# Kernel optimization log

Hardware: AMD Instinct MI355X
Metric: run time of the kernel (lower is better)

## Reference

```python
import jax, jax.numpy as jnp
import numpy as np

NUM_EMBEDDINGS = 1024
EMBEDDING_DIM = 256
COMMITMENT_COST = 0.25
B = 65536


def setup_inputs() -> dict:
    key = jax.random.key(0)
    k1, k2 = jax.random.split(key)
    inputs = jax.random.normal(k1, (B, EMBEDDING_DIM), dtype=jnp.float32)
    # torch init: uniform(-1/K, 1/K)
    W = jax.random.uniform(k2, (NUM_EMBEDDINGS, EMBEDDING_DIM), dtype=jnp.float32,
                           minval=-1.0 / NUM_EMBEDDINGS, maxval=1.0 / NUM_EMBEDDINGS)
    return {"inputs": inputs, "W": W}


def reference(inputs, W):
    x = inputs  # (B, D)
    # squared L2 distances to every codebook entry: (B, K)
    distances = (jnp.sum(x * x, axis=1, keepdims=True)
                 + jnp.sum(W * W, axis=1)
                 - 2.0 * jnp.matmul(x, W.T))
    idx = jnp.argmin(distances, axis=1)  # (B,)
    # one-hot @ W is just a gather
    quantized = jnp.take(W, idx, axis=0)  # (B, D)

    sg = jax.lax.stop_gradient
    e_latent_loss = jnp.mean((sg(quantized) - x) ** 2)
    q_latent_loss = jnp.mean((quantized - sg(x)) ** 2)
    loss = q_latent_loss + COMMITMENT_COST * e_latent_loss

    # perplexity from code-usage histogram (mean of one-hot rows)
    counts = jax.ops.segment_sum(jnp.ones((x.shape[0],), dtype=x.dtype), idx,
                                 num_segments=NUM_EMBEDDINGS)
    avg_probs = counts / x.shape[0]
    perplexity = jnp.exp(-jnp.sum(avg_probs * jnp.log(avg_probs + 1e-10)))

    # straight-through estimator
    quantized_st = x + sg(quantized - x)
    return quantized_st, loss, perplexity
```

## Files before the change

kernel.cpp:

```cpp
#include <hip/hip_runtime.h>


using h16   = _Float16;
using h16x8 = __attribute__((ext_vector_type(8))) _Float16;
using f32x4 = __attribute__((ext_vector_type(4))) float;

#define W_SCALE 1024.0f
#define W_UNSCALE2 0.001953125f
#define XS_STRIDE 264

__global__ __launch_bounds__(64) void vq_wconv(const float* __restrict__ W,
                                               h16* __restrict__ Whp,
                                               float* __restrict__ wws) {
  const int t = threadIdx.x;
  const int code = blockIdx.x * 2 + (t >> 5);
  const int j = t & 31;
  const int d0 = j * 8;
  f32x4 v0 = *(const f32x4*)(W + (size_t)code * 256 + d0);
  f32x4 v1 = *(const f32x4*)(W + (size_t)code * 256 + d0 + 4);
  h16x8 h;
  h[0] = (h16)(v0[0] * W_SCALE); h[1] = (h16)(v0[1] * W_SCALE);
  h[2] = (h16)(v0[2] * W_SCALE); h[3] = (h16)(v0[3] * W_SCALE);
  h[4] = (h16)(v1[0] * W_SCALE); h[5] = (h16)(v1[1] * W_SCALE);
  h[6] = (h16)(v1[2] * W_SCALE); h[7] = (h16)(v1[3] * W_SCALE);
  const int tile = code >> 4, ks = j >> 2, quad = j & 3, lm = code & 15;
  *(h16x8*)(Whp + (size_t)(((tile * 8 + ks) * 64 + quad * 16 + lm) * 8)) = h;
  float ss = v0[0] * v0[0] + v0[1] * v0[1] + v0[2] * v0[2] + v0[3] * v0[3]
           + v1[0] * v1[0] + v1[1] * v1[1] + v1[2] * v1[2] + v1[3] * v1[3];
#pragma unroll
  for (int m = 1; m <= 16; m <<= 1) ss += __shfl_xor(ss, m);
  if (j == 0) wws[code] = ss;
}

__global__ __launch_bounds__(256, 4) void vq_main(const float* __restrict__ X,
                                                  const h16* __restrict__ Whp,
                                                  const float* __restrict__ wws,
                                                  const float* __restrict__ W,
                                                  float* __restrict__ out,
                                                  float* __restrict__ loss_sum,
                                                  int* __restrict__ counts) {
  __shared__ h16 Xs[64 * XS_STRIDE];
  __shared__ float redS[4 * 64];
  __shared__ int redC[4 * 64];
  __shared__ int sIdx[64];
  __shared__ float xnorm[64];
  const int tid = threadIdx.x;
  const int lane = tid & 63;
  const int wid = tid >> 6;
  const int lm = lane & 15;
  const int quad = lane >> 4;
  const int rowBase = blockIdx.x * 64;

#pragma unroll
  for (int it = 0; it < 8; ++it) {
    int q = it * 256 + tid;
    int r = q >> 5;
    int dp = (q & 31) << 3;
    const float* src = X + (size_t)(rowBase + r) * 256 + dp;
    f32x4 v0 = __builtin_nontemporal_load((const f32x4*)src);
    f32x4 v1 = __builtin_nontemporal_load((const f32x4*)src + 1);
    h16x8 h;
    h[0] = (h16)v0[0]; h[1] = (h16)v0[1]; h[2] = (h16)v0[2]; h[3] = (h16)v0[3];
    h[4] = (h16)v1[0]; h[5] = (h16)v1[1]; h[6] = (h16)v1[2]; h[7] = (h16)v1[3];
    *(h16x8*)(Xs + r * XS_STRIDE + dp) = h;
    float ss = v0[0] * v0[0] + v0[1] * v0[1] + v0[2] * v0[2] + v0[3] * v0[3]
             + v1[0] * v1[0] + v1[1] * v1[1] + v1[2] * v1[2] + v1[3] * v1[3];
#pragma unroll
    for (int m = 1; m <= 16; m <<= 1) ss += __shfl_xor(ss, m);
    if ((q & 31) == 0) xnorm[r] = ss;
  }
  __syncthreads();

  float bestS[16];
  int bestC[16];
#pragma unroll
  for (int s = 0; s < 16; ++s) { bestS[s] = 3.4e38f; bestC[s] = 0x7fffffff; }

  for (int chunk = 0; chunk < 8; ++chunk) {
    const int tbase = chunk * 8 + wid * 2;
    const h16* bptr = Whp + (size_t)tbase * 4096 + lane * 8;
    float wn0 = wws[tbase * 16 + lm];
    float wn1 = wws[tbase * 16 + 16 + lm];
    f32x4 acc[4][2];
#pragma unroll
    for (int mt = 0; mt < 4; ++mt)
#pragma unroll
      for (int nt = 0; nt < 2; ++nt) {
        f32x4 z = {0.0f, 0.0f, 0.0f, 0.0f};
        acc[mt][nt] = z;
      }

#pragma unroll 2
    for (int ks = 0; ks < 8; ++ks) {
      h16x8 b0 = *(const h16x8*)(bptr + ks * 512);
      h16x8 b1 = *(const h16x8*)(bptr + ks * 512 + 4096);
      const int doff = ks * 32 + quad * 8;
#pragma unroll
      for (int mt = 0; mt < 4; ++mt) {
        h16x8 a = *(const h16x8*)(Xs + (mt * 16 + lm) * XS_STRIDE + doff);
        acc[mt][0] = __builtin_amdgcn_mfma_f32_16x16x32_f16(a, b0, acc[mt][0], 0, 0, 0);
        acc[mt][1] = __builtin_amdgcn_mfma_f32_16x16x32_f16(a, b1, acc[mt][1], 0, 0, 0);
      }
    }

#pragma unroll
    for (int nt = 0; nt < 2; ++nt) {
      int code = (tbase + nt) * 16 + lm;
      float wn = nt ? wn1 : wn0;
#pragma unroll
      for (int mt = 0; mt < 4; ++mt)
#pragma unroll
        for (int reg = 0; reg < 4; ++reg) {
          float s = fmaf(-W_UNSCALE2, acc[mt][nt][reg], wn);
          int slot = mt * 4 + reg;
          if (s < bestS[slot]) { bestS[slot] = s; bestC[slot] = code; }
        }
    }
  }

#pragma unroll
  for (int m = 1; m <= 8; m <<= 1) {
#pragma unroll
    for (int s = 0; s < 16; ++s) {
      float os = __shfl_xor(bestS[s], m);
      int oc = __shfl_xor(bestC[s], m);
      if (os < bestS[s] || (os == bestS[s] && oc < bestC[s])) { bestS[s] = os; bestC[s] = oc; }
    }
  }
  if (lm == 0) {
#pragma unroll
    for (int s = 0; s < 16; ++s) {
      int row = (s >> 2) * 16 + quad * 4 + (s & 3);
      redS[wid * 64 + row] = bestS[s];
      redC[wid * 64 + row] = bestC[s];
    }
  }
  __syncthreads();
  if (wid == 0) {
    float b = 3.4e38f;
    int c = 0x7fffffff;
#pragma unroll
    for (int w = 0; w < 4; ++w) {
      float s = redS[w * 64 + lane];
      int cc = redC[w * 64 + lane];
      if (s < b || (s == b && cc < c)) { b = s; c = cc; }
    }
    sIdx[lane] = c;
    atomicAdd(&counts[c], 1);
    float lossv = xnorm[lane] + b;
#pragma unroll
    for (int m = 1; m <= 32; m <<= 1) lossv += __shfl_xor(lossv, m);
    if (lane == 0) atomicAdd(loss_sum, lossv);
  }
  __syncthreads();

  const int d4 = lane << 2;
#pragma unroll 2
  for (int i = 0; i < 16; ++i) {
    int row = wid * 16 + i;
    int idx = sIdx[row];
    f32x4 qv = *(const f32x4*)(W + (size_t)idx * 256 + d4);
    __builtin_nontemporal_store(qv, (f32x4*)(out + (size_t)(rowBase + row) * 256 + d4));
  }
}

__global__ __launch_bounds__(256) void vq_finalize(const int* __restrict__ counts,
                                                   const float* __restrict__ loss_sum,
                                                   float* __restrict__ out) {
  __shared__ float red[256];
  const int tid = threadIdx.x;
  float h = 0.0f;
#pragma unroll
  for (int k = tid; k < 1024; k += 256) {
    float p = (float)counts[k] * (1.0f / 65536.0f);
    h += p * logf(p + 1e-10f);
  }
  red[tid] = h;
  __syncthreads();
#pragma unroll
  for (int s = 128; s > 0; s >>= 1) {
    if (tid < s) red[tid] += red[tid + s];
    __syncthreads();
  }
  if (tid == 0) {
    out[16777216] = loss_sum[0] * (1.25f / 16777216.0f);
    out[16777217] = expf(-red[0]);
  }
}

extern "C" void kernel_launch(void* const* d_in, const int* in_sizes, int n_in,
                              void* d_out, int out_size, void* d_ws, size_t ws_size,
                              hipStream_t stream) {
  (void)in_sizes; (void)n_in; (void)out_size; (void)ws_size;
  const float* X = (const float*)d_in[0];
  const float* W = (const float*)d_in[1];
  float* out = (float*)d_out;
  char* ws = (char*)d_ws;
  float* loss_sum = (float*)ws;
  int* counts = (int*)(ws + 256);
  float* wws = (float*)(ws + 4352);
  h16* Whp = (h16*)(ws + 8448);

  (void)hipMemsetAsync(d_ws, 0, 4352, stream);
  vq_wconv<<<512, 64, 0, stream>>>(W, Whp, wws);
  vq_main<<<1024, 256, 0, stream>>>(X, Whp, wws, W, out, loss_sum, counts);
  vq_finalize<<<1, 256, 0, stream>>>(counts, loss_sum, out);
}
```

Before: 179.4 us.

## Store X tile in MFMA fragment layout, fold memset into wconv, drop nontemporal hints

The X tile in shared memory is rearranged into a fragment-major layout, so each lane reads its A operand as one contiguous 16-byte chunk per (mt, ks). This is meant to reduce LDS bank conflicts and simplify address arithmetic. The workspace memset is removed and the zeroing is done by block 0 of the weight-conversion kernel, saving a separate launch. Nontemporal loads and stores are replaced by ordinary ones, which changes cache behaviour for the large X input and output streams.

Measured after the change: 169.0 us. 5.8% less time.

```diff
diff --git a/kernel.cpp b/kernel.cpp
--- a/kernel.cpp
+++ b/kernel.cpp
@@ -7,12 +7,17 @@
 
 #define W_SCALE 1024.0f
 #define W_UNSCALE2 0.001953125f
-#define XS_STRIDE 264
+#define FRAG_H 520
 
 __global__ __launch_bounds__(64) void vq_wconv(const float* __restrict__ W,
                                                h16* __restrict__ Whp,
-                                               float* __restrict__ wws) {
+                                               float* __restrict__ wws,
+                                               int* __restrict__ zero_base) {
   const int t = threadIdx.x;
+  if (blockIdx.x == 0) {
+#pragma unroll
+    for (int i = t; i < 1088; i += 64) zero_base[i] = 0;
+  }
   const int code = blockIdx.x * 2 + (t >> 5);
   const int j = t & 31;
   const int d0 = j * 8;
@@ -39,7 +44,7 @@
                                                   float* __restrict__ out,
                                                   float* __restrict__ loss_sum,
                                                   int* __restrict__ counts) {
-  __shared__ h16 Xs[64 * XS_STRIDE];
+  __shared__ h16 Xs[32 * FRAG_H];
   __shared__ float redS[4 * 64];
   __shared__ int redC[4 * 64];
   __shared__ int sIdx[64];
@@ -57,12 +62,13 @@
     int r = q >> 5;
     int dp = (q & 31) << 3;
     const float* src = X + (size_t)(rowBase + r) * 256 + dp;
-    f32x4 v0 = __builtin_nontemporal_load((const f32x4*)src);
-    f32x4 v1 = __builtin_nontemporal_load((const f32x4*)src + 1);
+    f32x4 v0 = *(const f32x4*)src;
+    f32x4 v1 = *(const f32x4*)(src + 4);
     h16x8 h;
     h[0] = (h16)v0[0]; h[1] = (h16)v0[1]; h[2] = (h16)v0[2]; h[3] = (h16)v0[3];
     h[4] = (h16)v1[0]; h[5] = (h16)v1[1]; h[6] = (h16)v1[2]; h[7] = (h16)v1[3];
-    *(h16x8*)(Xs + r * XS_STRIDE + dp) = h;
+    int mt = r >> 4, lmr = r & 15, ksw = dp >> 5, qdw = (dp >> 3) & 3;
+    *(h16x8*)(Xs + (mt * 8 + ksw) * FRAG_H + (qdw * 16 + lmr) * 8) = h;
     float ss = v0[0] * v0[0] + v0[1] * v0[1] + v0[2] * v0[2] + v0[3] * v0[3]
              + v1[0] * v1[0] + v1[1] * v1[1] + v1[2] * v1[2] + v1[3] * v1[3];
 #pragma unroll
@@ -78,7 +84,7 @@
 
   for (int chunk = 0; chunk < 8; ++chunk) {
     const int tbase = chunk * 8 + wid * 2;
-    const h16* bptr = Whp + (size_t)tbase * 4096 + lane * 8;
+    const h16* bp = Whp + (size_t)tbase * 4096 + lane * 8;
     float wn0 = wws[tbase * 16 + lm];
     float wn1 = wws[tbase * 16 + 16 + lm];
     f32x4 acc[4][2];
@@ -92,12 +98,11 @@
 
 #pragma unroll 2
     for (int ks = 0; ks < 8; ++ks) {
-      h16x8 b0 = *(const h16x8*)(bptr + ks * 512);
-      h16x8 b1 = *(const h16x8*)(bptr + ks * 512 + 4096);
-      const int doff = ks * 32 + quad * 8;
+      h16x8 b0 = *(const h16x8*)(bp + ks * 512);
+      h16x8 b1 = *(const h16x8*)(bp + ks * 512 + 4096);
 #pragma unroll
       for (int mt = 0; mt < 4; ++mt) {
-        h16x8 a = *(const h16x8*)(Xs + (mt * 16 + lm) * XS_STRIDE + doff);
+        h16x8 a = *(const h16x8*)(Xs + (mt * 8 + ks) * FRAG_H + lane * 8);
         acc[mt][0] = __builtin_amdgcn_mfma_f32_16x16x32_f16(a, b0, acc[mt][0], 0, 0, 0);
         acc[mt][1] = __builtin_amdgcn_mfma_f32_16x16x32_f16(a, b1, acc[mt][1], 0, 0, 0);
       }
@@ -160,7 +165,7 @@
     int row = wid * 16 + i;
     int idx = sIdx[row];
     f32x4 qv = *(const f32x4*)(W + (size_t)idx * 256 + d4);
-    __builtin_nontemporal_store(qv, (f32x4*)(out + (size_t)(rowBase + row) * 256 + d4));
+    *(f32x4*)(out + (size_t)(rowBase + row) * 256 + d4) = qv;
   }
 }
 
@@ -201,8 +206,7 @@
   float* wws = (float*)(ws + 4352);
   h16* Whp = (h16*)(ws + 8448);
 
-  (void)hipMemsetAsync(d_ws, 0, 4352, stream);
-  vq_wconv<<<512, 64, 0, stream>>>(W, Whp, wws);
+  vq_wconv<<<512, 64, 0, stream>>>(W, Whp, wws, (int*)ws);
   vq_main<<<1024, 256, 0, stream>>>(X, Whp, wws, W, out, loss_sum, counts);
   vq_finalize<<<1, 256, 0, stream>>>(counts, loss_sum, out);
 }
```
